# Kernel tuning notes

Measured on AMD Instinct MI355X. Metric: run time of the kernel, lower is better.

## Reference

```python
import jax, jax.numpy as jnp
import numpy as np
import math

B, L, CS, CZ = 1, 512, 256, 128
H, CH, PQ, PV = 8, 32, 4, 8
NUM_BLOCKS = 8
CAT = H * CH + H * PV * 3 + H * PV + H * CZ  # 1536


def _ln(x, g, b, eps=1e-5):
    mu = jnp.mean(x, -1, keepdims=True)
    var = jnp.mean((x - mu) ** 2, -1, keepdims=True)
    return (x - mu) * jax.lax.rsqrt(var + eps) * g + b


def _quat_to_rot(bq, cq, dq):
    # BackboneUpdate: quaternion with implicit a=1, normalized (AF2 Alg. 23)
    norm = jnp.sqrt(1.0 + bq * bq + cq * cq + dq * dq)
    a = 1.0 / norm
    b = bq / norm
    c = cq / norm
    d = dq / norm
    return jnp.stack([
        jnp.stack([a * a + b * b - c * c - d * d, 2 * (b * c - a * d), 2 * (b * d + a * c)], -1),
        jnp.stack([2 * (b * c + a * d), a * a - b * b + c * c - d * d, 2 * (c * d - a * b)], -1),
        jnp.stack([2 * (b * d - a * c), 2 * (c * d + a * b), a * a - b * b - c * c + d * d], -1),
    ], -2)


def _forward(s, z, mask, ln_s_g, ln_s_b, ln_z_g, ln_z_b, w_init, b_init,
             ln_ipa_g, ln_ipa_b, ln_tr_g, ln_tr_b,
             wq, bq, wk, bk, wv, bv, wqp, bqp, wkp, bkp, wvp, bvp,
             wpb, head_w, wo, bo, wt1, bt1, wt2, bt2, wt3, bt3, wbb, bbb):
    s0 = _ln(s, ln_s_g, ln_s_b)
    zn = _ln(z, ln_z_g, ln_z_b)
    sc = s0 @ w_init + b_init
    R = jnp.broadcast_to(jnp.eye(3, dtype=s.dtype), (B, L, 3, 3))
    t = jnp.zeros((B, L, 3), s.dtype)
    wL = math.sqrt(1.0 / 3.0)
    wC = math.sqrt(2.0 / (9.0 * PQ))
    gamma = jax.nn.softplus(head_w)  # [H]
    pair_bias = jnp.einsum('bijc,ch->bhij', zn, wpb)
    mask_bias = (mask[:, None, None, :] - 1.0) * 1e9
    for i in range(NUM_BLOCKS):
        # ---- Invariant Point Attention (AF2 Alg. 22, shared weights) ----
        q = (sc @ wq + bq).reshape(B, L, H, CH)
        k = (sc @ wk + bk).reshape(B, L, H, CH)
        v = (sc @ wv + bv).reshape(B, L, H, CH)
        qp = (sc @ wqp + bqp).reshape(B, L, H, PQ, 3)
        kp = (sc @ wkp + bkp).reshape(B, L, H, PQ, 3)
        vp = (sc @ wvp + bvp).reshape(B, L, H, PV, 3)
        tb = t[:, :, None, None, :]
        qpg = jnp.einsum('blij,blhpj->blhpi', R, qp) + tb  # local -> global
        kpg = jnp.einsum('blij,blhpj->blhpi', R, kp) + tb
        vpg = jnp.einsum('blij,blhpj->blhpi', R, vp) + tb
        scal = jnp.einsum('bihc,bjhc->bhij', q, k) / math.sqrt(CH)
        # sum_p ||qpg_i - kpg_j||^2 via |q|^2 + |k|^2 - 2 q.k (avoids [B,L,L,H,P,3])
        qk = jnp.einsum('bihpx,bjhpx->bhij', qpg, kpg)
        qn = jnp.moveaxis(jnp.sum(qpg ** 2, axis=(-2, -1)), -1, 1)  # [B,H,L]
        kn = jnp.moveaxis(jnp.sum(kpg ** 2, axis=(-2, -1)), -1, 1)
        d2 = qn[..., :, None] + kn[..., None, :] - 2.0 * qk  # [B,H,L,L]
        logits = wL * (scal + pair_bias - 0.5 * wC * gamma[None, :, None, None] * d2) + mask_bias
        a = jax.nn.softmax(logits, axis=-1)
        o = jnp.einsum('bhij,bjhc->bihc', a, v).reshape(B, L, H * CH)
        optg = jnp.einsum('bhij,bjhpx->bihpx', a, vpg)
        optl = jnp.einsum('blji,blhpj->blhpi', R, optg - tb)  # R^T (o - t)
        onrm = jnp.sqrt(jnp.sum(optl ** 2, -1) + 1e-8)  # [B,L,H,PV]
        opair = jnp.einsum('bhij,bijc->bihc', a, zn).reshape(B, L, H * CZ)
        cat = jnp.concatenate([o, optl.reshape(B, L, H * PV * 3), onrm.reshape(B, L, H * PV), opair], -1)
        ipa_up = cat @ wo + bo
        sc = _ln(sc + ipa_up, ln_ipa_g, ln_ipa_b)  # dropout = identity (eval)
        # ---- transition ----
        tr = jax.nn.relu(sc @ wt1 + bt1)
        tr = jax.nn.relu(tr @ wt2 + bt2)
        tr = (tr @ wt3 + bt3) * mask[..., None]
        sc = _ln(sc + tr, ln_tr_g, ln_tr_b)
        # ---- backbone update + frame composition ----
        upd = sc @ wbb + bbb  # [B,L,6]
        dR = _quat_to_rot(upd[..., 0], upd[..., 1], upd[..., 2])
        dt = upd[..., 3:6] * mask[..., None]
        t = jnp.einsum('blij,blj->bli', R, dt) + t
        R = jnp.einsum('blij,bljk->blik', R, dR)
        if i < NUM_BLOCKS - 1:
            R = jax.lax.stop_gradient(R)  # stop_rotation_gradients
    return sc, R, t


def setup_inputs() -> dict:
    key = jax.random.key(0)
    ks = jax.random.split(key, 20)
    w = lambda k, shape, sc=0.05: jax.random.normal(k, shape, jnp.float32) * sc
    inp = dict(
        s=jax.random.normal(ks[0], (B, L, CS), jnp.float32),
        z=jax.random.normal(ks[1], (B, L, L, CZ), jnp.float32),
        mask=jnp.ones((B, L), jnp.float32),
        ln_s_g=jnp.ones((CS,), jnp.float32), ln_s_b=jnp.zeros((CS,), jnp.float32),
        ln_z_g=jnp.ones((CZ,), jnp.float32), ln_z_b=jnp.zeros((CZ,), jnp.float32),
        w_init=w(ks[2], (CS, CS)), b_init=jnp.zeros((CS,), jnp.float32),
        ln_ipa_g=jnp.ones((CS,), jnp.float32), ln_ipa_b=jnp.zeros((CS,), jnp.float32),
        ln_tr_g=jnp.ones((CS,), jnp.float32), ln_tr_b=jnp.zeros((CS,), jnp.float32),
        wq=w(ks[3], (CS, H * CH)), bq=jnp.zeros((H * CH,), jnp.float32),
        wk=w(ks[4], (CS, H * CH)), bk=jnp.zeros((H * CH,), jnp.float32),
        wv=w(ks[5], (CS, H * CH)), bv=jnp.zeros((H * CH,), jnp.float32),
        wqp=w(ks[6], (CS, H * PQ * 3)), bqp=jnp.zeros((H * PQ * 3,), jnp.float32),
        wkp=w(ks[7], (CS, H * PQ * 3)), bkp=jnp.zeros((H * PQ * 3,), jnp.float32),
        wvp=w(ks[8], (CS, H * PV * 3)), bvp=jnp.zeros((H * PV * 3,), jnp.float32),
        wpb=w(ks[9], (CZ, H)),
        head_w=jnp.zeros((H,), jnp.float32),
        wo=w(ks[10], (CAT, CS), 0.02), bo=jnp.zeros((CS,), jnp.float32),
        wt1=w(ks[11], (CS, CS)), bt1=jnp.zeros((CS,), jnp.float32),
        wt2=w(ks[12], (CS, CS)), bt2=jnp.zeros((CS,), jnp.float32),
        wt3=w(ks[13], (CS, CS)), bt3=jnp.zeros((CS,), jnp.float32),
        wbb=w(ks[14], (CS, 6)), bbb=jnp.zeros((6,), jnp.float32),
    )
    return inp


def reference(s, z, mask, ln_s_g, ln_s_b, ln_z_g, ln_z_b, w_init, b_init,
              ln_ipa_g, ln_ipa_b, ln_tr_g, ln_tr_b,
              wq, bq, wk, bk, wv, bv, wqp, bqp, wkp, bkp, wvp, bvp,
              wpb, head_w, wo, bo, wt1, bt1, wt2, bt2, wt3, bt3, wbb, bbb):
    return _forward(s, z, mask, ln_s_g, ln_s_b, ln_z_g, ln_z_b, w_init, b_init,
                    ln_ipa_g, ln_ipa_b, ln_tr_g, ln_tr_b,
                    wq, bq, wk, bk, wv, bv, wqp, bqp, wkp, bkp, wvp, bvp,
                    wpb, head_w, wo, bo, wt1, bt1, wt2, bt2, wt3, bt3, wbb, bbb)
```

## Files before the change

kernel.cpp:

```cpp
#include <hip/hip_runtime.h>
#include <hip/hip_bf16.h>
#include <hip/hip_fp16.h>
#include <math.h>

#define Lq 512
#define CSd 256
#define CZd 128
#define Hd 8
#define CHd 32
#define PQd 4
#define PVd 8
#define CATd 1536
#define NPROJ 1152

typedef __attribute__((ext_vector_type(4))) float floatx4;
typedef __attribute__((ext_vector_type(8))) short shortx8;

#define OFF_SC      0
#define OFF_PB      393216
#define OFF_P       1441792
#define OFF_QN      2031616
#define OFF_KN      2035712
#define OFF_A16     2039808
#define OFF_CAT     4136960
#define OFF_S0      4923392
#define OFF_R       5054464
#define OFF_T       5059072
#define OFF_GAMMA   5060608
#define OFF_MASKB   5060616
#define OFF_BCAT    5061128
#define OFF_WINITP  5062280
#define OFF_WT1P    5127816
#define OFF_WT2P    5193352
#define OFF_WT3P    5258888
#define OFF_WOP     5324424
#define OFF_WCATP   5717640
#define OFF_QP      6012552
#define OFF_KP      6274696
#define OFF_VP      6536840
#define OFF_SCA16   6798984
#define OFF_ZNT     6930056

#define CAT_LO 786432

#define WLC 0.57735026918962576f
#define WCC 0.23570226039551584f
#define ISC 0.17677669529663687f

__device__ __forceinline__ float wave_sum(float v){
  #pragma unroll
  for (int m=32; m; m>>=1) v += __shfl_xor(v, m);
  return v;
}
__device__ __forceinline__ short f2bf(float v){
  __hip_bfloat16 h = (__hip_bfloat16)v;
  return __builtin_bit_cast(short, h);
}
__device__ __forceinline__ float bf2f(short s){
  unsigned u = ((unsigned)(unsigned short)s) << 16;
  return __builtin_bit_cast(float, u);
}
__device__ __forceinline__ __hip_bfloat16 s2b(short s){
  return __builtin_bit_cast(__hip_bfloat16, s);
}
__device__ __forceinline__ void cat_store(short* __restrict__ catA16, int k, int row, float v){
  size_t off = (((size_t)(k>>5)*512 + row)*4 + ((k>>3)&3))*8 + (k&7);
  short hh = f2bf(v);
  catA16[off]          = hh;
  catA16[off + CAT_LO] = f2bf(v - bf2f(hh));
}

__global__ __launch_bounds__(256) void k_setup(
    const float* __restrict__ bq, const float* __restrict__ bk, const float* __restrict__ bv,
    const float* __restrict__ bqp, const float* __restrict__ bkp, const float* __restrict__ bvp,
    const float* __restrict__ head_w, const float* __restrict__ mask,
    float* __restrict__ bcat, float* __restrict__ gamma,
    float* __restrict__ maskb, float* __restrict__ R, float* __restrict__ t){
  int k = blockIdx.x*256 + threadIdx.x;
  if (k < NPROJ){
    float v;
    if      (k < 256) v = bq[k];
    else if (k < 512) v = bk[k-256];
    else if (k < 768) v = bv[k-512];
    else if (k < 864) v = bqp[k-768];
    else if (k < 960) v = bkp[k-864];
    else              v = bvp[k-960];
    bcat[k] = v;
    return;
  }
  k -= NPROJ;
  if (k < Hd){ gamma[k] = log1pf(expf(head_w[k])); return; }
  k -= Hd;
  if (k < Lq){ maskb[k] = (mask[k] - 1.f)*1e9f; return; }
  k -= Lq;
  if (k < Lq){
    #pragma unroll
    for (int ii=0; ii<9; ii++) R[k*9+ii] = (ii==0||ii==4||ii==8) ? 1.f : 0.f;
    t[k*3] = 0.f; t[k*3+1] = 0.f; t[k*3+2] = 0.f;
  }
}

__global__ __launch_bounds__(256) void k_pack(
    const float* __restrict__ W, int K, int N, __hip_bfloat16* __restrict__ out){
  int idx = blockIdx.x*256 + threadIdx.x;
  if (idx >= K*N) return;
  int j = idx & 7, lane = (idx>>3) & 63, rest = idx >> 9;
  int nt = N >> 4;
  int tn = rest % nt, tk = rest / nt;
  int k = tk*32 + (lane>>4)*8 + j;
  int n = tn*16 + (lane&15);
  float v = W[(size_t)k*N + n];
  short h = f2bf(v);
  short l = f2bf(v - bf2f(h));
  size_t base = (size_t)rest*1024 + (idx & 511);
  out[base]       = s2b(h);
  out[base + 512] = s2b(l);
}

__global__ __launch_bounds__(256) void k_pack_cat(
    const float* __restrict__ wq, const float* __restrict__ wk, const float* __restrict__ wv,
    const float* __restrict__ wqp, const float* __restrict__ wkp, const float* __restrict__ wvp,
    __hip_bfloat16* __restrict__ out){
  int idx = blockIdx.x*256 + threadIdx.x;
  if (idx >= CSd*NPROJ) return;
  int j = idx & 7, lane = (idx>>3) & 63, rest = idx >> 9;
  const int nt = NPROJ >> 4;
  int tn = rest % nt, tk = rest / nt;
  int k = tk*32 + (lane>>4)*8 + j;
  int n = tn*16 + (lane&15);
  float v;
  if      (n < 256) v = wq[k*256 + n];
  else if (n < 512) v = wk[k*256 + n-256];
  else if (n < 768) v = wv[k*256 + n-512];
  else if (n < 864) v = wqp[k*96 + n-768];
  else if (n < 960) v = wkp[k*96 + n-864];
  else              v = wvp[k*192 + n-960];
  short h = f2bf(v);
  short l = f2bf(v - bf2f(h));
  size_t base = (size_t)rest*1024 + (idx & 511);
  out[base]       = s2b(h);
  out[base + 512] = s2b(l);
}

template<int NST>
__global__ __launch_bounds__(256) void k_gemm_mfma(
    const float* __restrict__ A, int K,
    const __hip_bfloat16* __restrict__ Bp, int N,
    const float* __restrict__ bias,
    float* __restrict__ Cf,
    int relu, const float* __restrict__ rowscale){
  int tid = threadIdx.x;
  int wave = tid>>6, lane = tid&63;
  int i0 = blockIdx.y*64 + wave*16;
  int n0 = blockIdx.x*(NST*16);
  int quad = lane>>4, l16 = lane&15;
  floatx4 acc[NST] = {};
  const int ntiles = N >> 4;
  const float* arow = A + (size_t)(i0 + l16)*K + quad*8;
  const __hip_bfloat16* bbase = Bp + ((size_t)(n0>>4))*1024 + (size_t)(lane&63)*8;
  for (int k0=0; k0<K; k0+=32){
    float4 v0 = *(const float4*)(arow + k0);
    float4 v1 = *(const float4*)(arow + k0 + 4);
    float av[8] = {v0.x,v0.y,v0.z,v0.w,v1.x,v1.y,v1.z,v1.w};
    shortx8 ahi, alo;
    #pragma unroll
    for (int j=0; j<8; j++){
      short h = f2bf(av[j]);
      ahi[j] = h;
      alo[j] = f2bf(av[j] - bf2f(h));
    }
    const __hip_bfloat16* bt = bbase + (size_t)(k0>>5)*ntiles*1024;
    #pragma unroll
    for (int s=0; s<NST; s++){
      shortx8 bhi = *(const shortx8*)(bt + s*1024);
      shortx8 blo = *(const shortx8*)(bt + s*1024 + 512);
      acc[s] = __builtin_amdgcn_mfma_f32_16x16x32_bf16(ahi, bhi, acc[s], 0, 0, 0);
      acc[s] = __builtin_amdgcn_mfma_f32_16x16x32_bf16(alo, bhi, acc[s], 0, 0, 0);
      acc[s] = __builtin_amdgcn_mfma_f32_16x16x32_bf16(ahi, blo, acc[s], 0, 0, 0);
    }
  }
  #pragma unroll
  for (int s=0; s<NST; s++){
    int n = n0 + s*16 + l16;
    float bs = bias ? bias[n] : 0.f;
    #pragma unroll
    for (int r=0; r<4; r++){
      int m = i0 + quad*4 + r;
      float v = acc[s][r] + bs;
      if (relu) v = fmaxf(v, 0.f);
      if (rowscale) v *= rowscale[m];
      Cf[(size_t)m*N + n] = v;
    }
  }
}

__global__ __launch_bounds__(256) void k_cvtA(
    const float* __restrict__ sc, short* __restrict__ scA16){
  int idx = blockIdx.x*256 + threadIdx.x;
  int i = idx>>5, c5 = idx&31;
  int c0 = c5*8, kc = c5>>2, quad = c5&3;
  float4 v0 = *(const float4*)(sc + (size_t)i*CSd + c0);
  float4 v1 = *(const float4*)(sc + (size_t)i*CSd + c0 + 4);
  float av[8] = {v0.x,v0.y,v0.z,v0.w,v1.x,v1.y,v1.z,v1.w};
  shortx8 hi, lo;
  #pragma unroll
  for (int j=0; j<8; j++){
    short h = f2bf(av[j]);
    hi[j] = h; lo[j] = f2bf(av[j] - bf2f(h));
  }
  size_t off = ((size_t)(kc*512 + i)*4 + quad)*8;
  *(shortx8*)(scA16 + off)          = hi;
  *(shortx8*)(scA16 + off + 131072) = lo;
}

__global__ __launch_bounds__(256) void k_gemm_proj(
    const short* __restrict__ scA16,
    const __hip_bfloat16* __restrict__ Bp,
    const float* __restrict__ bias,
    float* __restrict__ Cf){
  int tid = threadIdx.x;
  int wave = tid>>6, lane = tid&63;
  int i0 = blockIdx.y*64 + wave*16;
  int n0 = blockIdx.x*16;
  int quad = lane>>4, l16 = lane&15;
  floatx4 acc = {};
  const short* abase = scA16 + ((size_t)(i0 + l16)*4 + quad)*8;
  const __hip_bfloat16* bbase = Bp + (size_t)blockIdx.x*1024 + (size_t)lane*8;
  #pragma unroll
  for (int kc=0; kc<8; kc++){
    shortx8 ahi = *(const shortx8*)(abase + kc*16384);
    shortx8 alo = *(const shortx8*)(abase + kc*16384 + 131072);
    const __hip_bfloat16* bt = bbase + (size_t)kc*72*1024;
    shortx8 bhi = *(const shortx8*)bt;
    shortx8 blo = *(const shortx8*)(bt + 512);
    acc = __builtin_amdgcn_mfma_f32_16x16x32_bf16(ahi, bhi, acc, 0, 0, 0);
    acc = __builtin_amdgcn_mfma_f32_16x16x32_bf16(alo, bhi, acc, 0, 0, 0);
    acc = __builtin_amdgcn_mfma_f32_16x16x32_bf16(ahi, blo, acc, 0, 0, 0);
  }
  int n = n0 + l16;
  float bs = bias[n];
  #pragma unroll
  for (int r=0; r<4; r++)
    Cf[(size_t)(i0 + quad*4 + r)*NPROJ + n] = acc[r] + bs;
}

__global__ __launch_bounds__(256) void k_gemm_ipa(
    const short* __restrict__ catA16, const __hip_bfloat16* __restrict__ Bp,
    const float* __restrict__ bias, float* __restrict__ C){
  int tid = threadIdx.x;
  int wave = tid>>6, lane = tid&63;
  int ks = blockIdx.y >> 3;
  int i0 = (blockIdx.y & 7)*64 + wave*16;
  int n0 = blockIdx.x*16;
  int quad = lane>>4, l16 = lane&15;
  floatx4 acc = {};
  const short* abase = catA16 + (size_t)(ks*12)*16384 + (size_t)(i0 + l16)*32 + quad*8;
  const __hip_bfloat16* bbase = Bp + ((size_t)(ks*12*16 + blockIdx.x))*1024 + (size_t)lane*8;
  #pragma unroll
  for (int kc=0; kc<12; kc++){
    shortx8 ahi = *(const shortx8*)(abase + kc*16384);
    shortx8 alo = *(const shortx8*)(abase + kc*16384 + CAT_LO);
    const __hip_bfloat16* bt = bbase + (size_t)kc*16*1024;
    shortx8 bhi = *(const shortx8*)bt;
    shortx8 blo = *(const shortx8*)(bt + 512);
    acc = __builtin_amdgcn_mfma_f32_16x16x32_bf16(ahi, bhi, acc, 0, 0, 0);
    acc = __builtin_amdgcn_mfma_f32_16x16x32_bf16(alo, bhi, acc, 0, 0, 0);
    acc = __builtin_amdgcn_mfma_f32_16x16x32_bf16(ahi, blo, acc, 0, 0, 0);
  }
  float* Cp = C + (size_t)ks*131072;
  int n = n0 + l16;
  float bs = ks ? 0.f : bias[n];
  #pragma unroll
  for (int r=0; r<4; r++)
    Cp[(size_t)(i0 + quad*4 + r)*CSd + n] = acc[r] + bs;
}

__global__ __launch_bounds__(256) void k_addln(
    const float* __restrict__ x, const float* __restrict__ y,
    const float* __restrict__ g, const float* __restrict__ b,
    float* __restrict__ out){
  __shared__ float red[4];
  int row = blockIdx.x, tid = threadIdx.x;
  float v = x[row*CSd + tid];
  if (y) v += y[row*CSd + tid];
  int wid = tid>>6, lane = tid&63;
  float s = wave_sum(v);
  if (lane==0) red[wid] = s;
  __syncthreads();
  float mu = (red[0]+red[1]+red[2]+red[3]) * (1.f/CSd);
  __syncthreads();
  float d = v - mu;
  float s2 = wave_sum(d*d);
  if (lane==0) red[wid] = s2;
  __syncthreads();
  float var = (red[0]+red[1]+red[2]+red[3]) * (1.f/CSd);
  float rs = rsqrtf(var + 1e-5f);
  out[row*CSd + tid] = d*rs*g[tid] + b[tid];
}

__global__ __launch_bounds__(1024, 4) void k_lnz_pb(
    const float* __restrict__ z, const float* __restrict__ g, const float* __restrict__ b,
    const float* __restrict__ wpb, __half* __restrict__ pb, __hip_bfloat16* __restrict__ znt){
  __shared__ float Zt[64*129];
  __shared__ float wpbht[8*129];
  __shared__ float gl[128], bl[128];
  int tid = threadIdx.x;
  size_t row0 = (size_t)blockIdx.x*64;
  int ib = (int)(row0 >> 9), j0 = (int)(row0 & 511);
  {
    int c = tid>>3, h = tid&7;
    wpbht[h*129 + c] = wpb[tid];
  }
  if (tid < 128){ gl[tid] = g[tid]; bl[tid] = b[tid]; }
  {
    int w = tid>>6, lane = tid&63;
    #pragma unroll
    for (int it=0; it<4; it++){
      int row = it*16 + w;
      const float2 v = *(const float2*)(z + (row0+row)*(size_t)CZd + lane*2);
      Zt[row*129 + lane*2]     = v.x;
      Zt[row*129 + lane*2 + 1] = v.y;
    }
  }
  __syncthreads();
  {
    int r = tid>>4, q = tid&15;
    int rot = 2*(q>>2);
    float S1=0.f, S2=0.f;
    float zv[8];
    #pragma unroll
    for (int i=0; i<8; i++){
      int ii = (i + rot) & 7;
      float v = Zt[r*129 + q*8 + ii];
      zv[i] = v;
      S1 += v; S2 += v*v;
    }
    S1 += __shfl_xor(S1,1); S2 += __shfl_xor(S2,1);
    S1 += __shfl_xor(S1,2); S2 += __shfl_xor(S2,2);
    S1 += __shfl_xor(S1,4); S2 += __shfl_xor(S2,4);
    S1 += __shfl_xor(S1,8); S2 += __shfl_xor(S2,8);
    float mu = S1 * (1.f/128.f);
    float var = S2 * (1.f/128.f) - mu*mu;
    float rs = rsqrtf(var + 1e-5f);
    float d[8] = {};
    #pragma unroll
    for (int i=0; i<8; i++){
      int ii = (i + rot) & 7;
      int c = q*8 + ii;
      float znv = (zv[i]-mu)*rs*gl[c] + bl[c];
      Zt[r*129 + c] = znv;
      #pragma unroll
      for (int h=0; h<8; h++) d[h] += znv * wpbht[h*129 + c];
    }
    #pragma unroll
    for (int h=0; h<8; h++){
      d[h] += __shfl_xor(d[h],1);
      d[h] += __shfl_xor(d[h],2);
      d[h] += __shfl_xor(d[h],4);
      d[h] += __shfl_xor(d[h],8);
    }
    if (q == 0){
      #pragma unroll
      for (int h=0; h<8; h++)
        pb[((size_t)(h*Lq + ib))*Lq + j0 + r] = __float2half(d[h]);
    }
  }
  __syncthreads();
  {
    int c = tid>>3, jg = tid&7;
    int jb = jg*8;
    unsigned int o[4];
    #pragma unroll
    for (int k=0; k<4; k++){
      float z0 = Zt[(jb+2*k)*129 + c];
      float z1 = Zt[(jb+2*k+1)*129 + c];
      o[k] = ((unsigned int)(unsigned short)f2bf(z0)) |
             (((unsigned int)(unsigned short)f2bf(z1)) << 16);
    }
    unsigned short* zo = (unsigned short*)znt;
    uint4 pk = make_uint4(o[0],o[1],o[2],o[3]);
    *(uint4*)(zo + ((size_t)(ib*128 + c))*512 + j0 + jb) = pk;
  }
}

__global__ __launch_bounds__(256) void k_packqkv(
    const float* __restrict__ P, const float* __restrict__ R, const float* __restrict__ t,
    const float* __restrict__ gamma, int zfill,
    float* __restrict__ Qp, __hip_bfloat16* __restrict__ Kp, __hip_bfloat16* __restrict__ Vp,
    float* __restrict__ qn, float* __restrict__ kn){
  int idx = blockIdx.x*256 + threadIdx.x;
  int region = idx >> 15;
  int rem = idx & 32767;
  if (region == 0){
    int oct = rem & 7, h = (rem>>3)&7, j = rem>>6;
    float v[8] = {0.f,0.f,0.f,0.f,0.f,0.f,0.f,0.f};
    const float* Prow = P + (size_t)j*NPROJ;
    if (oct < 4){
      float4 a = *(const float4*)(Prow + 256 + h*CHd + oct*8);
      float4 b4 = *(const float4*)(Prow + 256 + h*CHd + oct*8 + 4);
      v[0]=a.x; v[1]=a.y; v[2]=a.z; v[3]=a.w; v[4]=b4.x; v[5]=b4.y; v[6]=b4.z; v[7]=b4.w;
    } else if (oct < 6){
      const float* kp = Prow + 864 + h*12;
      float4 k0 = *(const float4*)kp;
      float4 k1 = *(const float4*)(kp+4);
      float4 k2 = *(const float4*)(kp+8);
      float kv[12] = {k0.x,k0.y,k0.z,k0.w,k1.x,k1.y,k1.z,k1.w,k2.x,k2.y,k2.z,k2.w};
      float Rl[9];
      #pragma unroll
      for (int ii=0; ii<9; ii++) Rl[ii] = R[j*9+ii];
      float tv[3] = {t[j*3], t[j*3+1], t[j*3+2]};
      float gvals[12];
      #pragma unroll
      for (int p=0; p<4; p++)
        #pragma unroll
        for (int ax=0; ax<3; ax++)
          gvals[p*3+ax] = Rl[ax*3]*kv[p*3] + Rl[ax*3+1]*kv[p*3+1] + Rl[ax*3+2]*kv[p*3+2] + tv[ax];
      if (oct == 4){
        #pragma unroll
        for (int m=0; m<8; m++) v[m] = gvals[m];
      } else {
        #pragma unroll
        for (int m=0; m<4; m++) v[m] = gvals[8+m];
        float acc = 0.f;
        #pragma unroll
        for (int m=0; m<12; m++) acc += gvals[m]*gvals[m];
        kn[j*Hd + h] = acc;
      }
    } else {
      if (!zfill) return;
    }
    shortx8 hi, lo;
    #pragma unroll
    for (int m=0; m<8; m++){
      short hh = f2bf(v[m]);
      hi[m] = hh; lo[m] = f2bf(v[m] - bf2f(hh));
    }
    int kc = oct>>2, jt = j>>4, l16 = j&15, quad = oct&3;
    size_t base = (size_t)((h*2+kc)*32 + jt)*1024 + (quad*16+l16)*8;
    short* kp16 = (short*)Kp;
    *(shortx8*)(kp16 + base)       = hi;
    *(shortx8*)(kp16 + base + 512) = lo;
  } else if (region == 1){
    int n = rem & 63, h = (rem>>6)&7, jg = rem>>9;
    int jb = jg*8;
    float v[8] = {0.f,0.f,0.f,0.f,0.f,0.f,0.f,0.f};
    if (n < 32){
      #pragma unroll
      for (int m=0; m<8; m++) v[m] = P[(size_t)(jb+m)*NPROJ + 512 + h*CHd + n];
    } else if (n < 56){
      int p = (n-32)/3, ax = (n-32)%3;
      #pragma unroll
      for (int m=0; m<8; m++){
        int j = jb+m;
        const float* vp = P + (size_t)j*NPROJ + 960 + h*24 + p*3;
        const float* Rr = R + j*9 + ax*3;
        v[m] = Rr[0]*vp[0] + Rr[1]*vp[1] + Rr[2]*vp[2] + t[j*3+ax];
      }
    } else {
      if (!zfill) return;
    }
    shortx8 hi, lo;
    #pragma unroll
    for (int m=0; m<8; m++){
      short hh = f2bf(v[m]);
      hi[m] = hh; lo[m] = f2bf(v[m] - bf2f(hh));
    }
    int kc2 = jg>>2, w = n>>4, l16 = n&15, quad = jg&3;
    size_t base = (size_t)((h*16+kc2)*4 + w)*1024 + (quad*16+l16)*8;
    short* vp16 = (short*)Vp;
    *(shortx8*)(vp16 + base)       = hi;
    *(shortx8*)(vp16 + base + 512) = lo;
  } else {
    int oct = rem & 7, h = (rem>>3)&7, i = rem>>6;
    float v[8] = {0.f,0.f,0.f,0.f,0.f,0.f,0.f,0.f};
    const float* Prow = P + (size_t)i*NPROJ;
    if (oct < 4){
      float4 a = *(const float4*)(Prow + h*CHd + oct*8);
      float4 b4 = *(const float4*)(Prow + h*CHd + oct*8 + 4);
      const float sc = WLC*ISC;
      v[0]=a.x*sc; v[1]=a.y*sc; v[2]=a.z*sc; v[3]=a.w*sc;
      v[4]=b4.x*sc; v[5]=b4.y*sc; v[6]=b4.z*sc; v[7]=b4.w*sc;
    } else if (oct < 6){
      const float* qp = Prow + 768 + h*12;
      float4 k0 = *(const float4*)qp;
      float4 k1 = *(const float4*)(qp+4);
      float4 k2 = *(const float4*)(qp+8);
      float kv[12] = {k0.x,k0.y,k0.z,k0.w,k1.x,k1.y,k1.z,k1.w,k2.x,k2.y,k2.z,k2.w};
      float Rl[9];
      #pragma unroll
      for (int ii=0; ii<9; ii++) Rl[ii] = R[i*9+ii];
      float tv[3] = {t[i*3], t[i*3+1], t[i*3+2]};
      float gvals[12];
      #pragma unroll
      for (int p=0; p<4; p++)
        #pragma unroll
        for (int ax=0; ax<3; ax++)
          gvals[p*3+ax] = Rl[ax*3]*kv[p*3] + Rl[ax*3+1]*kv[p*3+1] + Rl[ax*3+2]*kv[p*3+2] + tv[ax];
      float sc = WLC*WCC*gamma[h];
      if (oct == 4){
        #pragma unroll
        for (int m=0; m<8; m++) v[m] = gvals[m]*sc;
      } else {
        #pragma unroll
        for (int m=0; m<4; m++) v[m] = gvals[8+m]*sc;
        float acc = 0.f;
        #pragma unroll
        for (int m=0; m<12; m++) acc += gvals[m]*gvals[m];
        qn[i*Hd + h] = acc;
      }
    } else {
      if (!zfill) return;
    }
    float* qrow = Qp + ((size_t)h*512 + i)*64 + oct*8;
    *(float4*)qrow       = make_float4(v[0],v[1],v[2],v[3]);
    *(float4*)(qrow + 4) = make_float4(v[4],v[5],v[6],v[7]);
  }
}

__global__ __launch_bounds__(1024) void k_attn(
    const float* __restrict__ Qp, const __hip_bfloat16* __restrict__ Kp,
    const __hip_bfloat16* __restrict__ Vp,
    const float* __restrict__ qn, const float* __restrict__ kn,
    const __half* __restrict__ pb, const float* __restrict__ maskb,
    const float* __restrict__ gamma,
    const float* __restrict__ R, const float* __restrict__ t,
    __hip_bfloat16* __restrict__ a16hi,
    short* __restrict__ catA16){
  __shared__ float At[16][516];
  __shared__ short AbfH[16*4*16*8];
  __shared__ short AbfL[16*4*16*8];
  __shared__ float Pv[3][16][68];
  __shared__ float Ot[16][36];
  __shared__ float qnL[16];
  int tid = threadIdx.x;
  int i0 = blockIdx.x*16, h = blockIdx.y;
  int wave = tid>>6, lane = tid&63, quad = lane>>4, l16 = lane&15;
  int kg = wave>>2, ng = wave&3;
  float gam = gamma[h];
  float coef = 0.5f*WLC*WCC*gam;
  if (tid < 16) qnL[tid] = qn[(i0+tid)*Hd + h];
  __syncthreads();
  const float* qrow = Qp + ((size_t)h*512 + i0 + l16)*64 + quad*8;
  shortx8 qhi[2], qlo[2];
  #pragma unroll
  for (int kc=0; kc<2; kc++){
    float4 v0 = *(const float4*)(qrow + kc*32);
    float4 v1 = *(const float4*)(qrow + kc*32 + 4);
    float av[8] = {v0.x,v0.y,v0.z,v0.w,v1.x,v1.y,v1.z,v1.w};
    #pragma unroll
    for (int j=0; j<8; j++){
      short hh = f2bf(av[j]);
      qhi[kc][j] = hh; qlo[kc][j] = f2bf(av[j] - bf2f(hh));
    }
  }
  #pragma unroll
  for (int it=0; it<2; it++){
    int jt = it*16 + wave;
    floatx4 acc = {};
    #pragma unroll
    for (int kc=0; kc<2; kc++){
      const __hip_bfloat16* bt = Kp + (size_t)((h*2+kc)*32 + jt)*1024 + lane*8;
      shortx8 bhi = *(const shortx8*)bt;
      shortx8 blo = *(const shortx8*)(bt + 512);
      acc = __builtin_amdgcn_mfma_f32_16x16x32_bf16(qhi[kc], bhi, acc, 0, 0, 0);
      acc = __builtin_amdgcn_mfma_f32_16x16x32_bf16(qlo[kc], bhi, acc, 0, 0, 0);
      acc = __builtin_amdgcn_mfma_f32_16x16x32_bf16(qhi[kc], blo, acc, 0, 0, 0);
    }
    int j = jt*16 + l16;
    float knj = kn[j*Hd + h];
    float mbj = maskb[j];
    #pragma unroll
    for (int r=0; r<4; r++){
      int i = quad*4 + r;
      float pbv = __half2float(pb[((size_t)(h*Lq) + i0 + i)*Lq + j]);
      At[i][j] = acc[r] + WLC*pbv + mbj - coef*(qnL[i] + knj);
    }
  }
  __syncthreads();
  {
    int w = wave;
    float v[8];
    float m = -1e30f;
    #pragma unroll
    for (int k=0; k<8; k++){ v[k] = At[w][lane + 64*k]; m = fmaxf(m, v[k]); }
    #pragma unroll
    for (int msk=32; msk; msk>>=1) m = fmaxf(m, __shfl_xor(m, msk));
    float ssum = 0.f;
    #pragma unroll
    for (int k=0; k<8; k++){ float e = __expf(v[k]-m); v[k]=e; ssum += e; }
    #pragma unroll
    for (int msk=32; msk; msk>>=1) ssum += __shfl_xor(ssum, msk);
    float inv = 1.f/ssum;
    #pragma unroll
    for (int k=0; k<8; k++){
      int cc = lane + 64*k;
      float p = v[k]*inv;
      short hh = f2bf(p);
      short ll = f2bf(p - bf2f(hh));
      a16hi[(((size_t)(i0+w)*16 + (cc>>5))*8 + h)*32 + (cc&31)] = s2b(hh);
      int off = ((((cc>>5)*4 + ((cc>>3)&3))*16 + w)<<3) + (cc&7);
      AbfH[off] = hh;
      AbfL[off] = ll;
    }
  }
  __syncthreads();
  floatx4 acc2 = {};
  #pragma unroll
  for (int kk=0; kk<4; kk++){
    int kc2 = kg*4 + kk;
    int aoff = (((kc2*4 + quad)*16 + l16))<<3;
    shortx8 ahi = *(const shortx8*)&AbfH[aoff];
    shortx8 alo = *(const shortx8*)&AbfL[aoff];
    const __hip_bfloat16* bt = Vp + (size_t)((h*16+kc2)*4 + ng)*1024 + lane*8;
    shortx8 bhi = *(const shortx8*)bt;
    shortx8 blo = *(const shortx8*)(bt + 512);
    acc2 = __builtin_amdgcn_mfma_f32_16x16x32_bf16(ahi, bhi, acc2, 0, 0, 0);
    acc2 = __builtin_amdgcn_mfma_f32_16x16x32_bf16(alo, bhi, acc2, 0, 0, 0);
    acc2 = __builtin_amdgcn_mfma_f32_16x16x32_bf16(ahi, blo, acc2, 0, 0, 0);
  }
  if (kg > 0){
    #pragma unroll
    for (int r=0;r<4;r++) Pv[kg-1][quad*4+r][ng*16+l16] = acc2[r];
  }
  __syncthreads();
  if (kg == 0){
    int n = ng*16 + l16;
    #pragma unroll
    for (int r=0;r<4;r++){
      int i = quad*4+r;
      float v = acc2[r] + Pv[0][i][n] + Pv[1][i][n] + Pv[2][i][n];
      if (n < 32) cat_store(catA16, h*CHd + n, i0+i, v);
      else        Ot[i][n-32] = v;
    }
  }
  __syncthreads();
  if (tid < 128){
    int i = tid>>3, p = tid&7, gi = i0+i;
    float o0 = Ot[i][p*3], o1 = Ot[i][p*3+1], o2 = Ot[i][p*3+2];
    float d0 = o0 - t[gi*3], d1 = o1 - t[gi*3+1], d2 = o2 - t[gi*3+2];
    const float* Rm = R + gi*9;
    float l0 = Rm[0]*d0 + Rm[3]*d1 + Rm[6]*d2;
    float l1 = Rm[1]*d0 + Rm[4]*d1 + Rm[7]*d2;
    float l2 = Rm[2]*d0 + Rm[5]*d1 + Rm[8]*d2;
    int kb = 256 + h*24 + p*3;
    cat_store(catA16, kb,   gi, l0);
    cat_store(catA16, kb+1, gi, l1);
    cat_store(catA16, kb+2, gi, l2);
    cat_store(catA16, 448 + h*8 + p, gi, sqrtf(l0*l0 + l1*l1 + l2*l2 + 1e-8f));
  }
}

__global__ __launch_bounds__(512) void k_opair_mfma(
    const __hip_bfloat16* __restrict__ a16hi,
    const __hip_bfloat16* __restrict__ znt, short* __restrict__ catA16){
  int i = blockIdx.x;
  int tid = threadIdx.x;
  int wave = tid>>6, lane = tid&63, quad = lane>>4, l16 = lane&15;
  int nt = wave;
  floatx4 acc = {};
  const __hip_bfloat16* abase_h = a16hi + ((size_t)i*16*8 + (l16&7))*32 + quad*8;
  const __hip_bfloat16* zb = znt + ((size_t)i*128 + nt*16 + l16)*512 + quad*8;
  #pragma unroll
  for (int kt=0; kt<16; kt++){
    shortx8 ah = *(const shortx8*)(abase_h + kt*256);
    shortx8 b0 = *(const shortx8*)(zb + kt*32);
    acc = __builtin_amdgcn_mfma_f32_16x16x32_bf16(ah, b0, acc, 0, 0, 0);
  }
  if (quad < 2){
    #pragma unroll
    for (int r=0; r<4; r++){
      int h = quad*4 + r;
      cat_store(catA16, 512 + h*CZd + nt*16 + l16, i, acc[r]);
    }
  }
}

__device__ __forceinline__ void gemm_bf16w(
    const short* __restrict__ AHp, const short* __restrict__ ALp,
    short* __restrict__ OH, short* __restrict__ OL, float (*Yf)[260],
    const __hip_bfloat16* __restrict__ Wp, const float* __restrict__ bias,
    bool relu, int tid){
  int wave = tid>>6, lane = tid&63, quad = lane>>4, l16 = lane&15;
  floatx4 acc = {};
  #pragma unroll
  for (int kc=0; kc<8; kc++){
    int aoff = (((kc*4 + quad)*16 + l16))<<3;
    shortx8 ahi = *(const shortx8*)&AHp[aoff];
    shortx8 alo = *(const shortx8*)&ALp[aoff];
    const __hip_bfloat16* bt = Wp + (size_t)(kc*16 + wave)*1024 + lane*8;
    shortx8 bhi = *(const shortx8*)bt;
    shortx8 blo = *(const shortx8*)(bt + 512);
    acc = __builtin_amdgcn_mfma_f32_16x16x32_bf16(ahi, bhi, acc, 0, 0, 0);
    acc = __builtin_amdgcn_mfma_f32_16x16x32_bf16(alo, bhi, acc, 0, 0, 0);
    acc = __builtin_amdgcn_mfma_f32_16x16x32_bf16(ahi, blo, acc, 0, 0, 0);
  }
  int n = wave*16 + l16;
  float bs = bias[n];
  #pragma unroll
  for (int r=0;r<4;r++){
    float v = acc[r] + bs;
    if (relu) v = fmaxf(v, 0.f);
    int row = quad*4 + r;
    if (OH){
      short hh = f2bf(v);
      int off = ((((n>>5)*4 + ((n>>3)&3))*16 + row)<<3) + (n&7);
      OH[off] = hh;
      OL[off] = f2bf(v - bf2f(hh));
    } else {
      Yf[row][n] = v;
    }
  }
}

__global__ __launch_bounds__(1024) void k_mega(
    float* __restrict__ scb, const float* __restrict__ ipa,
    const float* __restrict__ gi_, const float* __restrict__ bi_,
    const __hip_bfloat16* __restrict__ W1, const float* __restrict__ c1,
    const __hip_bfloat16* __restrict__ W2, const float* __restrict__ c2,
    const __hip_bfloat16* __restrict__ W3, const float* __restrict__ c3,
    const float* __restrict__ gt_, const float* __restrict__ bt_,
    const float* __restrict__ mask,
    const float* __restrict__ wbb, const float* __restrict__ bbb,
    float* __restrict__ R, float* __restrict__ t, short* __restrict__ scA16){
  __shared__ float As[16][260], Bs[16][260];
  __shared__ short AH[2][4096], AL[2][4096];
  __shared__ float rA[16][33], rB[16][33];
  __shared__ float mv[16][2];
  __shared__ float u6p[16][6][2];
  int tid = threadIdx.x;
  int i0 = blockIdx.x*16;
  int r = (tid>>5)&15, c5 = tid&31, c0 = c5*8;
  float v[8];
  if (tid < 512){
    const float* sr = scb + (size_t)(i0+r)*CSd + c0;
    const float* p0 = ipa + (size_t)(i0+r)*CSd + c0;
    const float* p1 = p0 + 131072;
    const float* p2 = p0 + 262144;
    const float* p3 = p0 + 393216;
    float s1=0.f, s2=0.f;
    #pragma unroll
    for (int k2=0;k2<8;k2++){
      float x = sr[k2] + p0[k2] + p1[k2] + p2[k2] + p3[k2];
      v[k2]=x; s1+=x; s2+=x*x;
    }
    rA[r][c5]=s1; rB[r][c5]=s2;
  }
  __syncthreads();
  if (tid<16){
    float s1=0.f,s2=0.f;
    #pragma unroll
    for (int c=0;c<32;c++){ s1+=rA[tid][c]; s2+=rB[tid][c]; }
    float mu = s1*(1.f/CSd), var = s2*(1.f/CSd) - mu*mu;
    mv[tid][0]=mu; mv[tid][1]=rsqrtf(var+1e-5f);
  }
  __syncthreads();
  if (tid < 512){
    float mu=mv[r][0], rs=mv[r][1];
    #pragma unroll
    for (int k2=0;k2<8;k2++){
      int col = c0+k2;
      float o = (v[k2]-mu)*rs*gi_[col] + bi_[col];
      As[r][col] = o;
      short hh = f2bf(o);
      int off = ((((col>>5)*4 + ((col>>3)&3))*16 + r)<<3) + (col&7);
      AH[0][off] = hh;
      AL[0][off] = f2bf(o - bf2f(hh));
    }
  }
  __syncthreads();
  gemm_bf16w(AH[0], AL[0], AH[1], AL[1], nullptr, W1, c1, true, tid);
  __syncthreads();
  gemm_bf16w(AH[1], AL[1], AH[0], AL[0], nullptr, W2, c2, true, tid);
  __syncthreads();
  gemm_bf16w(AH[0], AL[0], nullptr, nullptr, Bs, W3, c3, false, tid);
  __syncthreads();
  if (tid < 512){
    float mk = mask[i0+r];
    float s1=0.f, s2=0.f;
    #pragma unroll
    for (int k2=0;k2<8;k2++){ float x = As[r][c0+k2] + Bs[r][c0+k2]*mk; v[k2]=x; s1+=x; s2+=x*x; }
    rA[r][c5]=s1; rB[r][c5]=s2;
  }
  __syncthreads();
  if (tid<16){
    float s1=0.f,s2=0.f;
    #pragma unroll
    for (int c=0;c<32;c++){ s1+=rA[tid][c]; s2+=rB[tid][c]; }
    float mu = s1*(1.f/CSd), var = s2*(1.f/CSd) - mu*mu;
    mv[tid][0]=mu; mv[tid][1]=rsqrtf(var+1e-5f);
  }
  __syncthreads();
  if (tid < 512){
    float mu=mv[r][0], rs=mv[r][1];
    float* out = scb + (size_t)(i0+r)*CSd + c0;
    shortx8 hi, lo;
    #pragma unroll
    for (int k2=0;k2<8;k2++){
      int col = c0+k2;
      float o = (v[k2]-mu)*rs*gt_[col] + bt_[col];
      As[r][col] = o;
      out[k2] = o;
      short hh = f2bf(o);
      hi[k2] = hh; lo[k2] = f2bf(o - bf2f(hh));
    }
    size_t off = ((size_t)((c5>>2)*512 + i0 + r)*4 + (c5&3))*8;
    *(shortx8*)(scA16 + off)          = hi;
    *(shortx8*)(scA16 + off + 131072) = lo;
  }
  __syncthreads();
  if (tid < 192){
    int rr = tid/12, o = (tid%12)>>1, half = tid&1;
    float acc = half ? 0.f : bbb[o];
    int kb = half*128;
    for (int k2=kb; k2<kb+128; k2++) acc += As[rr][k2]*wbb[k2*6+o];
    u6p[rr][o][half] = acc;
  }
  __syncthreads();
  if (tid < 16){
    int gidx = i0 + tid;
    float uu[6];
    #pragma unroll
    for (int o=0;o<6;o++) uu[o] = u6p[tid][o][0] + u6p[tid][o][1];
    float bq = uu[0], cq = uu[1], dq = uu[2];
    float norm = sqrtf(1.f + bq*bq + cq*cq + dq*dq);
    float a = 1.f/norm, b_ = bq/norm, c_ = cq/norm, d_ = dq/norm;
    float dR[9];
    dR[0] = a*a + b_*b_ - c_*c_ - d_*d_; dR[1] = 2.f*(b_*c_ - a*d_); dR[2] = 2.f*(b_*d_ + a*c_);
    dR[3] = 2.f*(b_*c_ + a*d_); dR[4] = a*a - b_*b_ + c_*c_ - d_*d_; dR[5] = 2.f*(c_*d_ - a*b_);
    dR[6] = 2.f*(b_*d_ - a*c_); dR[7] = 2.f*(c_*d_ + a*b_); dR[8] = a*a - b_*b_ - c_*c_ + d_*d_;
    float mk = mask[gidx];
    float dt0 = uu[3]*mk, dt1 = uu[4]*mk, dt2 = uu[5]*mk;
    float Rm[9];
    #pragma unroll
    for (int ii=0; ii<9; ii++) Rm[ii] = R[gidx*9+ii];
    t[gidx*3]   += Rm[0]*dt0 + Rm[1]*dt1 + Rm[2]*dt2;
    t[gidx*3+1] += Rm[3]*dt0 + Rm[4]*dt1 + Rm[5]*dt2;
    t[gidx*3+2] += Rm[6]*dt0 + Rm[7]*dt1 + Rm[8]*dt2;
    #pragma unroll
    for (int ii=0; ii<3; ii++)
      #pragma unroll
      for (int jj=0; jj<3; jj++)
        R[gidx*9 + ii*3 + jj] = Rm[ii*3]*dR[jj] + Rm[ii*3+1]*dR[3+jj] + Rm[ii*3+2]*dR[6+jj];
  }
}

__global__ __launch_bounds__(256) void k_writeout(
    const float* __restrict__ sc, const float* __restrict__ R, const float* __restrict__ t,
    float* __restrict__ out){
  int idx = blockIdx.x*256 + threadIdx.x;
  if      (idx < 131072) out[idx] = sc[idx];
  else if (idx < 135680) out[idx] = R[idx-131072];
  else if (idx < 137216) out[idx] = t[idx-135680];
}

extern "C" void kernel_launch(void* const* d_in, const int* in_sizes, int n_in,
                              void* d_out, int out_size, void* d_ws, size_t ws_size,
                              hipStream_t stream){
  const float* s      = (const float*)d_in[0];
  const float* z      = (const float*)d_in[1];
  const float* mask   = (const float*)d_in[2];
  const float* ln_s_g = (const float*)d_in[3];
  const float* ln_s_b = (const float*)d_in[4];
  const float* ln_z_g = (const float*)d_in[5];
  const float* ln_z_b = (const float*)d_in[6];
  const float* w_init = (const float*)d_in[7];
  const float* b_init = (const float*)d_in[8];
  const float* ln_ipa_g = (const float*)d_in[9];
  const float* ln_ipa_b = (const float*)d_in[10];
  const float* ln_tr_g  = (const float*)d_in[11];
  const float* ln_tr_b  = (const float*)d_in[12];
  const float* wq = (const float*)d_in[13]; const float* bq = (const float*)d_in[14];
  const float* wk = (const float*)d_in[15]; const float* bk = (const float*)d_in[16];
  const float* wv = (const float*)d_in[17]; const float* bv = (const float*)d_in[18];
  const float* wqp = (const float*)d_in[19]; const float* bqp = (const float*)d_in[20];
  const float* wkp = (const float*)d_in[21]; const float* bkp = (const float*)d_in[22];
  const float* wvp = (const float*)d_in[23]; const float* bvp = (const float*)d_in[24];
  const float* wpb = (const float*)d_in[25];
  const float* head_w = (const float*)d_in[26];
  const float* wo = (const float*)d_in[27]; const float* bo = (const float*)d_in[28];
  const float* wt1 = (const float*)d_in[29]; const float* bt1 = (const float*)d_in[30];
  const float* wt2 = (const float*)d_in[31]; const float* bt2 = (const float*)d_in[32];
  const float* wt3 = (const float*)d_in[33]; const float* bt3 = (const float*)d_in[34];
  const float* wbb = (const float*)d_in[35]; const float* bbb = (const float*)d_in[36];

  float* W = (float*)d_ws;
  float* scb   = W + OFF_SC;
  __half*  pbb  = (__half*)(W + OFF_PB);
  float* Pb    = W + OFF_P;
  float* qnb   = W + OFF_QN;
  float* knb   = W + OFF_KN;
  __hip_bfloat16* a16hi = (__hip_bfloat16*)(W + OFF_A16);
  short* catA16 = (short*)(W + OFF_CAT);
  float* s0b   = W + OFF_S0;
  float* Rb    = W + OFF_R;
  float* tb    = W + OFF_T;
  float* gammab= W + OFF_GAMMA;
  float* maskb = W + OFF_MASKB;
  float* bcat  = W + OFF_BCAT;
  __hip_bfloat16* WinitP = (__hip_bfloat16*)(W + OFF_WINITP);
  __hip_bfloat16* Wt1P   = (__hip_bfloat16*)(W + OFF_WT1P);
  __hip_bfloat16* Wt2P   = (__hip_bfloat16*)(W + OFF_WT2P);
  __hip_bfloat16* Wt3P   = (__hip_bfloat16*)(W + OFF_WT3P);
  __hip_bfloat16* WoP    = (__hip_bfloat16*)(W + OFF_WOP);
  __hip_bfloat16* WcatP  = (__hip_bfloat16*)(W + OFF_WCATP);
  float* Qp = W + OFF_QP;
  __hip_bfloat16* Kp = (__hip_bfloat16*)(W + OFF_KP);
  __hip_bfloat16* Vp = (__hip_bfloat16*)(W + OFF_VP);
  short* scA16 = (short*)(W + OFF_SCA16);
  __hip_bfloat16* znt = (__hip_bfloat16*)(W + OFF_ZNT);

  k_setup<<<9, 256, 0, stream>>>(bq,bk,bv,bqp,bkp,bvp, head_w, mask, bcat, gammab, maskb, Rb, tb);
  k_pack_cat<<<CSd*NPROJ/256, 256, 0, stream>>>(wq,wk,wv,wqp,wkp,wvp, WcatP);
  k_pack<<<256,  256, 0, stream>>>(w_init, CSd, CSd, WinitP);
  k_pack<<<1536, 256, 0, stream>>>(wo, CATd, CSd, WoP);
  k_pack<<<256,  256, 0, stream>>>(wt1, CSd, CSd, Wt1P);
  k_pack<<<256,  256, 0, stream>>>(wt2, CSd, CSd, Wt2P);
  k_pack<<<256,  256, 0, stream>>>(wt3, CSd, CSd, Wt3P);

  k_addln<<<Lq, 256, 0, stream>>>(s, nullptr, ln_s_g, ln_s_b, s0b);
  k_gemm_mfma<4><<<dim3(4,8), 256, 0, stream>>>(s0b, CSd, WinitP, CSd, b_init, scb, 0, nullptr);
  k_cvtA<<<64, 256, 0, stream>>>(scb, scA16);
  k_lnz_pb<<<Lq*Lq/64, 1024, 0, stream>>>(z, ln_z_g, ln_z_b, wpb, pbb, znt);

  for (int it=0; it<8; ++it){
    k_gemm_proj<<<dim3(72,8), 256, 0, stream>>>(scA16, WcatP, bcat, Pb);
    k_packqkv<<<384, 256, 0, stream>>>(Pb, Rb, tb, gammab, (it==0)?1:0,
                                       Qp, Kp, Vp, qnb, knb);
    k_attn<<<dim3(32,8), 1024, 0, stream>>>(Qp, Kp, Vp, qnb, knb, pbb, maskb, gammab, Rb, tb,
                                            a16hi, catA16);
    k_opair_mfma<<<Lq, 512, 0, stream>>>(a16hi, znt, catA16);
    k_gemm_ipa<<<dim3(16,32), 256, 0, stream>>>(catA16, WoP, bo, Pb);
    k_mega<<<32, 1024, 0, stream>>>(scb, Pb, ln_ipa_g, ln_ipa_b,
                                    Wt1P, bt1, Wt2P, bt2, Wt3P, bt3,
                                    ln_tr_g, ln_tr_b, mask, wbb, bbb, Rb, tb, scA16);
  }
  k_writeout<<<536, 256, 0, stream>>>(scb, Rb, tb, (float*)d_out);
}
```

Before: 832.9 us.

## Halve attention block size, alias its shared buffers, and merge weight packing kernels

The attention kernel now runs with 512 threads instead of 1024. Each wave handles more key tiles, two softmax rows and twice as many PV k-chunks, so the cross-wave partial-sum buffer shrinks. The score matrix and the bf16 hi/lo probability buffers share one aliased shared-memory region, with an extra barrier between the softmax reduction and the writes that overwrite it. This cuts LDS use and may allow more blocks per CU. The six weight-packing launches are merged into one kernel to save launch overhead in setup.

```diff
diff --git a/kernel.cpp b/kernel.cpp
--- a/kernel.cpp
+++ b/kernel.cpp
@@ -100,10 +100,8 @@
   }
 }
 
-__global__ __launch_bounds__(256) void k_pack(
-    const float* __restrict__ W, int K, int N, __hip_bfloat16* __restrict__ out){
-  int idx = blockIdx.x*256 + threadIdx.x;
-  if (idx >= K*N) return;
+__device__ __forceinline__ void pack_one(
+    const float* __restrict__ W, int N, __hip_bfloat16* __restrict__ out, int idx){
   int j = idx & 7, lane = (idx>>3) & 63, rest = idx >> 9;
   int nt = N >> 4;
   int tn = rest % nt, tk = rest / nt;
@@ -117,29 +115,45 @@
   out[base + 512] = s2b(l);
 }
 
-__global__ __launch_bounds__(256) void k_pack_cat(
+__global__ __launch_bounds__(256) void k_packall(
     const float* __restrict__ wq, const float* __restrict__ wk, const float* __restrict__ wv,
     const float* __restrict__ wqp, const float* __restrict__ wkp, const float* __restrict__ wvp,
-    __hip_bfloat16* __restrict__ out){
+    const float* __restrict__ w_init, const float* __restrict__ wo,
+    const float* __restrict__ wt1, const float* __restrict__ wt2, const float* __restrict__ wt3,
+    __hip_bfloat16* __restrict__ WcatP, __hip_bfloat16* __restrict__ WinitP,
+    __hip_bfloat16* __restrict__ WoP, __hip_bfloat16* __restrict__ Wt1P,
+    __hip_bfloat16* __restrict__ Wt2P, __hip_bfloat16* __restrict__ Wt3P){
   int idx = blockIdx.x*256 + threadIdx.x;
-  if (idx >= CSd*NPROJ) return;
-  int j = idx & 7, lane = (idx>>3) & 63, rest = idx >> 9;
-  const int nt = NPROJ >> 4;
-  int tn = rest % nt, tk = rest / nt;
-  int k = tk*32 + (lane>>4)*8 + j;
-  int n = tn*16 + (lane&15);
-  float v;
-  if      (n < 256) v = wq[k*256 + n];
-  else if (n < 512) v = wk[k*256 + n-256];
-  else if (n < 768) v = wv[k*256 + n-512];
-  else if (n < 864) v = wqp[k*96 + n-768];
-  else if (n < 960) v = wkp[k*96 + n-864];
-  else              v = wvp[k*192 + n-960];
-  short h = f2bf(v);
-  short l = f2bf(v - bf2f(h));
-  size_t base = (size_t)rest*1024 + (idx & 511);
-  out[base]       = s2b(h);
-  out[base + 512] = s2b(l);
+  if (idx < CSd*NPROJ){
+    int j = idx & 7, lane = (idx>>3) & 63, rest = idx >> 9;
+    const int nt = NPROJ >> 4;
+    int tn = rest % nt, tk = rest / nt;
+    int k = tk*32 + (lane>>4)*8 + j;
+    int n = tn*16 + (lane&15);
+    float v;
+    if      (n < 256) v = wq[k*256 + n];
+    else if (n < 512) v = wk[k*256 + n-256];
+    else if (n < 768) v = wv[k*256 + n-512];
+    else if (n < 864) v = wqp[k*96 + n-768];
+    else if (n < 960) v = wkp[k*96 + n-864];
+    else              v = wvp[k*192 + n-960];
+    short h = f2bf(v);
+    short l = f2bf(v - bf2f(h));
+    size_t base = (size_t)rest*1024 + (idx & 511);
+    WcatP[base]       = s2b(h);
+    WcatP[base + 512] = s2b(l);
+    return;
+  }
+  idx -= CSd*NPROJ;
+  if (idx < CSd*CSd){ pack_one(w_init, CSd, WinitP, idx); return; }
+  idx -= CSd*CSd;
+  if (idx < CATd*CSd){ pack_one(wo, CSd, WoP, idx); return; }
+  idx -= CATd*CSd;
+  if (idx < CSd*CSd){ pack_one(wt1, CSd, Wt1P, idx); return; }
+  idx -= CSd*CSd;
+  if (idx < CSd*CSd){ pack_one(wt2, CSd, Wt2P, idx); return; }
+  idx -= CSd*CSd;
+  if (idx < CSd*CSd){ pack_one(wt3, CSd, Wt3P, idx); return; }
 }
 
 template<int NST>
@@ -517,7 +531,7 @@
   }
 }
 
-__global__ __launch_bounds__(1024) void k_attn(
+__global__ __launch_bounds__(512) void k_attn(
     const float* __restrict__ Qp, const __hip_bfloat16* __restrict__ Kp,
     const __hip_bfloat16* __restrict__ Vp,
     const float* __restrict__ qn, const float* __restrict__ kn,
@@ -526,12 +540,14 @@
     const float* __restrict__ R, const float* __restrict__ t,
     __hip_bfloat16* __restrict__ a16hi,
     short* __restrict__ catA16){
-  __shared__ float At[16][516];
-  __shared__ short AbfH[16*4*16*8];
-  __shared__ short AbfL[16*4*16*8];
-  __shared__ float Pv[3][16][68];
+  __shared__ char sbuf[16*516*4];
+  __shared__ float Pv[16][68];
   __shared__ float Ot[16][36];
   __shared__ float qnL[16];
+  float (*At)[516] = (float(*)[516])sbuf;
+  short* AbfH = (short*)sbuf;
+  short* AbfL = (short*)(sbuf + 16384*2);
+  AbfL = (short*)(sbuf + 16384);
   int tid = threadIdx.x;
   int i0 = blockIdx.x*16, h = blockIdx.y;
   int wave = tid>>6, lane = tid&63, quad = lane>>4, l16 = lane&15;
@@ -554,8 +570,8 @@
     }
   }
   #pragma unroll
-  for (int it=0; it<2; it++){
-    int jt = it*16 + wave;
+  for (int it=0; it<4; it++){
+    int jt = it*8 + wave;
     floatx4 acc = {};
     #pragma unroll
     for (int kc=0; kc<2; kc++){
@@ -577,28 +593,35 @@
     }
   }
   __syncthreads();
-  {
-    int w = wave;
-    float v[8];
+  float va[2][8];
+  float inv[2];
+  #pragma unroll
+  for (int rr2=0; rr2<2; rr2++){
+    int rr = wave + rr2*8;
     float m = -1e30f;
     #pragma unroll
-    for (int k=0; k<8; k++){ v[k] = At[w][lane + 64*k]; m = fmaxf(m, v[k]); }
+    for (int k=0; k<8; k++){ va[rr2][k] = At[rr][lane + 64*k]; m = fmaxf(m, va[rr2][k]); }
     #pragma unroll
     for (int msk=32; msk; msk>>=1) m = fmaxf(m, __shfl_xor(m, msk));
     float ssum = 0.f;
     #pragma unroll
-    for (int k=0; k<8; k++){ float e = __expf(v[k]-m); v[k]=e; ssum += e; }
+    for (int k=0; k<8; k++){ float e = __expf(va[rr2][k]-m); va[rr2][k]=e; ssum += e; }
     #pragma unroll
     for (int msk=32; msk; msk>>=1) ssum += __shfl_xor(ssum, msk);
-    float inv = 1.f/ssum;
+    inv[rr2] = 1.f/ssum;
+  }
+  __syncthreads();
+  #pragma unroll
+  for (int rr2=0; rr2<2; rr2++){
+    int rr = wave + rr2*8;
     #pragma unroll
     for (int k=0; k<8; k++){
       int cc = lane + 64*k;
-      float p = v[k]*inv;
+      float p = va[rr2][k]*inv[rr2];
       short hh = f2bf(p);
       short ll = f2bf(p - bf2f(hh));
-      a16hi[(((size_t)(i0+w)*16 + (cc>>5))*8 + h)*32 + (cc&31)] = s2b(hh);
-      int off = ((((cc>>5)*4 + ((cc>>3)&3))*16 + w)<<3) + (cc&7);
+      a16hi[(((size_t)(i0+rr)*16 + (cc>>5))*8 + h)*32 + (cc&31)] = s2b(hh);
+      int off = ((((cc>>5)*4 + ((cc>>3)&3))*16 + rr)<<3) + (cc&7);
       AbfH[off] = hh;
       AbfL[off] = ll;
     }
@@ -606,8 +629,8 @@
   __syncthreads();
   floatx4 acc2 = {};
   #pragma unroll
-  for (int kk=0; kk<4; kk++){
-    int kc2 = kg*4 + kk;
+  for (int kk=0; kk<8; kk++){
+    int kc2 = kg*8 + kk;
     int aoff = (((kc2*4 + quad)*16 + l16))<<3;
     shortx8 ahi = *(const shortx8*)&AbfH[aoff];
     shortx8 alo = *(const shortx8*)&AbfL[aoff];
@@ -618,9 +641,9 @@
     acc2 = __builtin_amdgcn_mfma_f32_16x16x32_bf16(alo, bhi, acc2, 0, 0, 0);
     acc2 = __builtin_amdgcn_mfma_f32_16x16x32_bf16(ahi, blo, acc2, 0, 0, 0);
   }
-  if (kg > 0){
-    #pragma unroll
-    for (int r=0;r<4;r++) Pv[kg-1][quad*4+r][ng*16+l16] = acc2[r];
+  if (kg == 1){
+    #pragma unroll
+    for (int r=0;r<4;r++) Pv[quad*4+r][ng*16+l16] = acc2[r];
   }
   __syncthreads();
   if (kg == 0){
@@ -628,7 +651,7 @@
     #pragma unroll
     for (int r=0;r<4;r++){
       int i = quad*4+r;
-      float v = acc2[r] + Pv[0][i][n] + Pv[1][i][n] + Pv[2][i][n];
+      float v = acc2[r] + Pv[i][n];
       if (n < 32) cat_store(catA16, h*CHd + n, i0+i, v);
       else        Ot[i][n-32] = v;
     }
@@ -910,12 +933,8 @@
   __hip_bfloat16* znt = (__hip_bfloat16*)(W + OFF_ZNT);
 
   k_setup<<<9, 256, 0, stream>>>(bq,bk,bv,bqp,bkp,bvp, head_w, mask, bcat, gammab, maskb, Rb, tb);
-  k_pack_cat<<<CSd*NPROJ/256, 256, 0, stream>>>(wq,wk,wv,wqp,wkp,wvp, WcatP);
-  k_pack<<<256,  256, 0, stream>>>(w_init, CSd, CSd, WinitP);
-  k_pack<<<1536, 256, 0, stream>>>(wo, CATd, CSd, WoP);
-  k_pack<<<256,  256, 0, stream>>>(wt1, CSd, CSd, Wt1P);
-  k_pack<<<256,  256, 0, stream>>>(wt2, CSd, CSd, Wt2P);
-  k_pack<<<256,  256, 0, stream>>>(wt3, CSd, CSd, Wt3P);
+  k_packall<<<3712, 256, 0, stream>>>(wq,wk,wv,wqp,wkp,wvp, w_init, wo, wt1, wt2, wt3,
+                                      WcatP, WinitP, WoP, Wt1P, Wt2P, Wt3P);
 
   k_addln<<<Lq, 256, 0, stream>>>(s, nullptr, ln_s_g, ln_s_b, s0b);
   k_gemm_mfma<4><<<dim3(4,8), 256, 0, stream>>>(s0b, CSd, WinitP, CSd, b_init, scb, 0, nullptr);
@@ -926,8 +945,8 @@
     k_gemm_proj<<<dim3(72,8), 256, 0, stream>>>(scA16, WcatP, bcat, Pb);
     k_packqkv<<<384, 256, 0, stream>>>(Pb, Rb, tb, gammab, (it==0)?1:0,
                                        Qp, Kp, Vp, qnb, knb);
-    k_attn<<<dim3(32,8), 1024, 0, stream>>>(Qp, Kp, Vp, qnb, knb, pbb, maskb, gammab, Rb, tb,
-                                            a16hi, catA16);
+    k_attn<<<dim3(32,8), 512, 0, stream>>>(Qp, Kp, Vp, qnb, knb, pbb, maskb, gammab, Rb, tb,
+                                           a16hi, catA16);
     k_opair_mfma<<<Lq, 512, 0, stream>>>(a16hi, znt, catA16);
     k_gemm_ipa<<<dim3(16,32), 256, 0, stream>>>(catA16, WoP, bo, Pb);
     k_mega<<<32, 1024, 0, stream>>>(scb, Pb, ln_ipa_g, ln_ipa_b,
```

Result: no change. 820.5 us (-1.5%).
